# Performance work log

Measured on AMD Instinct MI355X. Metric: run time of the kernel, lower is better.

The kernel has to match this reference:

```python
import jax, jax.numpy as jnp
import numpy as np

N = 50000      # nodes
E = 500000     # directed edges
F_IN = 112     # node feature dim
G = 256        # number of graphs in batch


def _lin(key, fan_in, fan_out):
    # torch nn.Linear default init: U(-1/sqrt(fan_in), 1/sqrt(fan_in))
    s = 1.0 / np.sqrt(fan_in)
    kw, kb = jax.random.split(key)
    W = jax.random.uniform(kw, (fan_in, fan_out), jnp.float32, -s, s)
    b = jax.random.uniform(kb, (fan_out,), jnp.float32, -s, s)
    return W, b


def setup_inputs() -> dict:
    key = jax.random.key(0)
    ks = jax.random.split(key, 9)
    x = jax.random.normal(ks[0], (N, F_IN), jnp.float32)
    edge_index = jax.random.randint(ks[1], (2, E), 0, N)
    # sorted graph ids, guaranteeing every graph id 0..G-1 appears
    batch = jnp.sort(jnp.concatenate([jnp.arange(G),
                                      jax.random.randint(ks[2], (N - G,), 0, G)]))
    W1, b1 = _lin(ks[3], F_IN, 336)
    W2, b2 = _lin(ks[4], 336, 168)
    Wg, bg = _lin(ks[5], 168, 84)
    Wf, bf = _lin(ks[6], 84, 42)
    Wo, bo = _lin(ks[7], 42, 1)
    return dict(x=x, edge_index=edge_index, batch=batch,
                W1=W1, b1=b1, W2=W2, b2=b2,
                Wg=Wg, bg=bg, Wf=Wf, bf=bf, Wo=Wo, bo=bo)


def _gcn_conv(x, W, b, src, dst, n):
    """PyG GCNConv: add self-loops, symmetric D^-1/2 A D^-1/2 normalization."""
    h = x @ W                                   # [n, out]
    loop = jnp.arange(n, dtype=src.dtype)
    src_f = jnp.concatenate([src, loop])        # [E+n]
    dst_f = jnp.concatenate([dst, loop])
    deg = jax.ops.segment_sum(jnp.ones(src_f.shape[0], jnp.float32), dst_f, n)
    dinv = jnp.where(deg > 0, jax.lax.rsqrt(deg), 0.0)
    norm = dinv[src_f] * dinv[dst_f]            # [E+n]
    out = jax.ops.segment_sum(h[src_f] * norm[:, None], dst_f, n)
    return out + b


def reference(x, edge_index, batch, W1, b1, W2, b2, Wg, bg, Wf, bf, Wo, bo):
    src, dst = edge_index[0], edge_index[1]
    h = jax.nn.relu(_gcn_conv(x, W1, b1, src, dst, N))
    # dropout is identity in eval mode
    h = jax.nn.relu(_gcn_conv(h, W2, b2, src, dst, N))
    g = jax.ops.segment_max(h, batch, G)        # global max pool -> [G, 168]
    g = jax.nn.relu(g @ Wg + bg)
    g = jax.nn.relu(g @ Wf + bf)
    return g @ Wo + bo                           # [G, 1]
```

## Files before the change

### kernel.cpp

```cpp
#include <hip/hip_runtime.h>
#include <hip/hip_fp16.h>

#define N_NODES 50000
#define MPAD    50048
#define N_EDGES 500000
#define F_IN    112
#define K1P     128
#define F1      336
#define K2P     352
#define F2      168
#define NGRAPH  256
#define SCAN_CHUNK 1024
#define SCAN_BLOCKS ((N_NODES + SCAN_CHUNK - 1) / SCAN_CHUNK)

typedef __attribute__((ext_vector_type(8))) _Float16 f16x8;
typedef __attribute__((ext_vector_type(4))) float f32x4;
typedef unsigned short ushort_t;

__device__ __forceinline__ ushort_t f16_bits(float x) {
    __half h = __float2half_rn(x);
    return *(ushort_t*)&h;
}

__global__ void k_zero_int(int* p, int n) {
    int i = blockIdx.x * blockDim.x + threadIdx.x;
    if (i < n) p[i] = 0;
}

#define CVX_BLOCKS  ((N_NODES * (F_IN / 4) + 255) / 256)
#define CNT_BLOCKS  ((N_EDGES / 2 + 255) / 256)
#define CVW1_BLOCKS ((384 * K1P + 255) / 256)
#define CVW2_BLOCKS ((192 * K2P + 255) / 256)
#define RNG_BLOCKS  ((N_NODES + 255) / 256)
#define PREP_BLOCKS (CVX_BLOCKS + CNT_BLOCKS + CVW1_BLOCKS + CVW2_BLOCKS + RNG_BLOCKS)

__global__ __launch_bounds__(256) void k_prep(const float* __restrict__ x,
                                              const int* __restrict__ dst,
                                              const float* __restrict__ W1,
                                              const float* __restrict__ W2,
                                              const int* __restrict__ batch,
                                              ushort_t* __restrict__ x16,
                                              int* __restrict__ dcount,
                                              ushort_t* __restrict__ w1t,
                                              ushort_t* __restrict__ w2t,
                                              int* __restrict__ r0, int* __restrict__ r1) {
    int bid = blockIdx.x;
    int t = threadIdx.x;
    if (bid < CVX_BLOCKS) {
        int i = bid * 256 + t;
        if (i < N_NODES * (F_IN / 4)) {
            float4 v = ((const float4*)x)[i];
            __half2 h0 = __floats2half2_rn(v.x, v.y);
            __half2 h1 = __floats2half2_rn(v.z, v.w);
            uint2 u; u.x = *(unsigned*)&h0; u.y = *(unsigned*)&h1;
            ((uint2*)x16)[i] = u;
        }
        return;
    }
    bid -= CVX_BLOCKS;
    if (bid < CNT_BLOCKS) {
        int i = bid * 256 + t;
        if (i < N_EDGES / 2) {
            int2 d = ((const int2*)dst)[i];
            atomicAdd(&dcount[d.x], 1);
            atomicAdd(&dcount[d.y], 1);
        }
        return;
    }
    bid -= CNT_BLOCKS;
    if (bid < CVW1_BLOCKS) {
        int idx = bid * 256 + t;
        if (idx < 384 * K1P) {
            int n = idx / K1P, k = idx % K1P;
            float v = (n < F1 && k < F_IN) ? W1[k * F1 + n] : 0.0f;
            w1t[idx] = f16_bits(v);
        }
        return;
    }
    bid -= CVW1_BLOCKS;
    if (bid < CVW2_BLOCKS) {
        int idx = bid * 256 + t;
        if (idx < 192 * K2P) {
            int n = idx / K2P, k = idx % K2P;
            float v = (n < F2 && k < F1) ? W2[k * F2 + n] : 0.0f;
            w2t[idx] = f16_bits(v);
        }
        return;
    }
    bid -= CVW2_BLOCKS;
    {
        int v = bid * 256 + t;
        if (v >= N_NODES) return;
        int b = batch[v];
        if (v == 0 || batch[v - 1] != b) r0[b] = v;
        if (v == N_NODES - 1 || batch[v + 1] != b) r1[b] = v + 1;
    }
}

__global__ __launch_bounds__(SCAN_CHUNK) void k_scan1(const int* __restrict__ dcount,
                                                      int* __restrict__ off,
                                                      int* __restrict__ partials,
                                                      float* __restrict__ dinv, int n) {
    __shared__ int s[SCAN_CHUNK];
    int t = threadIdx.x;
    int i = blockIdx.x * SCAN_CHUNK + t;
    int val = (i < n) ? dcount[i] : 0;
    s[t] = val;
    __syncthreads();
    for (int d = 1; d < SCAN_CHUNK; d <<= 1) {
        int x = (t >= d) ? s[t - d] : 0;
        __syncthreads();
        s[t] += x;
        __syncthreads();
    }
    if (i < n) {
        off[i] = s[t] - val;
        dinv[i] = rsqrtf((float)val + 1.0f);
    }
    if (t == SCAN_CHUNK - 1) partials[blockIdx.x] = s[t];
}
__global__ __launch_bounds__(SCAN_CHUNK) void k_scan3(int* __restrict__ off,
                                                      const int* __restrict__ partials, int n) {
    __shared__ int tmp[SCAN_BLOCKS];
    __shared__ int pref[SCAN_BLOCKS];
    int t = threadIdx.x;
    if (t < SCAN_BLOCKS) tmp[t] = partials[t];
    __syncthreads();
    if (t == 0) {
        int run = 0;
        for (int j = 0; j < SCAN_BLOCKS; ++j) { pref[j] = run; run += tmp[j]; }
    }
    __syncthreads();
    int i = blockIdx.x * SCAN_CHUNK + t;
    if (i < n) off[i] += pref[blockIdx.x];
    if (i == n) off[i] = N_EDGES;
}

__global__ void k_scatter(const int* __restrict__ src, const int* __restrict__ dst,
                          const int* __restrict__ off, int* __restrict__ cur,
                          const float* __restrict__ dinv,
                          int2* __restrict__ csr, int e2) {
    int i = blockIdx.x * blockDim.x + threadIdx.x;
    if (i >= e2) return;
    int2 s2 = ((const int2*)src)[i];
    int2 d2 = ((const int2*)dst)[i];
    {
        int pos = atomicAdd(&cur[d2.x], 1);
        int2 rec; rec.x = s2.x; rec.y = __float_as_int(dinv[s2.x] * dinv[d2.x]);
        csr[off[d2.x] + pos] = rec;
    }
    {
        int pos = atomicAdd(&cur[d2.y], 1);
        int2 rec; rec.x = s2.y; rec.y = __float_as_int(dinv[s2.y] * dinv[d2.y]);
        csr[off[d2.y] + pos] = rec;
    }
}

__global__ __launch_bounds__(256) void k_agg1(const ushort_t* __restrict__ X16,
                                              const int* __restrict__ off,
                                              const int2* __restrict__ csr,
                                              const float* __restrict__ dinv,
                                              ushort_t* __restrict__ aX) {
    int w = (blockIdx.x * 256 + threadIdx.x) >> 6;
    int lane = threadIdx.x & 63;
    if (w >= N_NODES / 2) return;
    const int g = lane >> 5, sl = lane & 31;
    const int v = 2 * w + g;
    const bool act = sl < 28;
    int o0A = off[2 * w], oM = off[2 * w + 1], o1B = off[2 * w + 2];
    int o0 = g ? oM : o0A;
    int n  = g ? (o1B - oM) : (oM - o0A);
    int nmax = max(oM - o0A, o1B - oM);
    float di = dinv[v];
    float4 acc = {0, 0, 0, 0};
    if (act) {
        uint2 u = *(const uint2*)(X16 + (long)v * F_IN + sl * 4);
        float2 f0 = __half22float2(*(__half2*)&u.x);
        float2 f1 = __half22float2(*(__half2*)&u.y);
        float s2 = di * di;
        acc.x = f0.x * s2; acc.y = f0.y * s2; acc.z = f1.x * s2; acc.w = f1.y * s2;
    }
    int nm1 = max(n - 1, 0);
    for (int b = 0; b < nmax; b += 8) {
        int2 e[8];
        #pragma unroll
        for (int j = 0; j < 8; ++j) {
            int cidx = min(o0 + min(b + j, nm1), N_EDGES - 1);
            e[j] = csr[cidx];
        }
        uint2 u[8];
        #pragma unroll
        for (int j = 0; j < 8; ++j) {
            bool valid = (b + j) < n;
            int s = valid ? e[j].x : v;
            if (act) u[j] = *(const uint2*)(X16 + (long)s * F_IN + sl * 4);
        }
        #pragma unroll
        for (int j = 0; j < 8; ++j) {
            bool valid = (b + j) < n;
            float c = valid ? __int_as_float(e[j].y) : 0.0f;
            float2 f0 = __half22float2(*(__half2*)&u[j].x);
            float2 f1 = __half22float2(*(__half2*)&u[j].y);
            acc.x += c * f0.x; acc.y += c * f0.y; acc.z += c * f1.x; acc.w += c * f1.y;
        }
    }
    if (sl < 32) {
        uint2 o = {0, 0};
        if (act) {
            __half2 h0 = __floats2half2_rn(acc.x, acc.y);
            __half2 h1 = __floats2half2_rn(acc.z, acc.w);
            o.x = *(unsigned*)&h0; o.y = *(unsigned*)&h1;
        }
        *(uint2*)(aX + (long)v * K1P + sl * 4) = o;
    }
}

template<int NT, int KP, int EPI>
__global__ __launch_bounds__(256) void k_gemm_f16(
        const ushort_t* __restrict__ A, const ushort_t* __restrict__ Bt,
        const float* __restrict__ bias,
        ushort_t* __restrict__ C, int M, int Nreal, int CW) {
    constexpr int NS = NT / 32;
    __shared__ ushort_t As[64][40];
    __shared__ ushort_t Bs[NT][40];
    const int tid = threadIdx.x;
    const int row0 = blockIdx.y * 64;
    const int col0 = blockIdx.x * NT;
    const int w  = tid >> 6, l = tid & 63;
    const int wm = w >> 1, wn = w & 1;
    const int lm = l & 15, lq = l >> 4;

    f32x4 acc[2][NS];
    #pragma unroll
    for (int i = 0; i < 2; ++i)
        #pragma unroll
        for (int j = 0; j < NS; ++j) acc[i][j] = (f32x4){0.f, 0.f, 0.f, 0.f};

    const int arow  = tid >> 2;
    const int akoff = (tid & 3) * 8;

    for (int k0 = 0; k0 < KP; k0 += 32) {
        *(int4*)&As[arow][akoff] = *(const int4*)&A[(long)(row0 + arow) * KP + k0 + akoff];
        #pragma unroll
        for (int c = 0; c < NT / 64; ++c)
            *(int4*)&Bs[c * 64 + arow][akoff] =
                *(const int4*)&Bt[(long)(col0 + c * 64 + arow) * KP + k0 + akoff];
        __syncthreads();

        f16x8 af[2], bf[NS];
        #pragma unroll
        for (int ms = 0; ms < 2; ++ms)
            af[ms] = *(const f16x8*)&As[wm * 32 + ms * 16 + lm][lq * 8];
        #pragma unroll
        for (int ns = 0; ns < NS; ++ns)
            bf[ns] = *(const f16x8*)&Bs[wn * (NT / 2) + ns * 16 + lm][lq * 8];
        #pragma unroll
        for (int ms = 0; ms < 2; ++ms)
            #pragma unroll
            for (int ns = 0; ns < NS; ++ns)
                acc[ms][ns] = __builtin_amdgcn_mfma_f32_16x16x32_f16(af[ms], bf[ns], acc[ms][ns], 0, 0, 0);
        __syncthreads();
    }

    #pragma unroll
    for (int ms = 0; ms < 2; ++ms) {
        int R = row0 + wm * 32 + ms * 16 + lq * 4;
        #pragma unroll
        for (int ns = 0; ns < NS; ++ns) {
            int col = col0 + wn * (NT / 2) + ns * 16 + lm;
            if (EPI == 1) {
                if (col < CW) {
                    float bb = (col < Nreal) ? bias[col] : 0.0f;
                    #pragma unroll
                    for (int i = 0; i < 4; ++i) {
                        int row = R + i;
                        if (row < M) {
                            float r = (col < Nreal) ? fmaxf(acc[ms][ns][i] + bb, 0.0f) : 0.0f;
                            C[(long)row * CW + col] = f16_bits(r);
                        }
                    }
                }
            } else {
                if (col < Nreal) {
                    #pragma unroll
                    for (int i = 0; i < 4; ++i) {
                        int row = R + i;
                        if (row < M) C[(long)row * Nreal + col] = f16_bits(acc[ms][ns][i]);
                    }
                }
            }
        }
    }
}

__global__ __launch_bounds__(256) void k_agg2(const ushort_t* __restrict__ T16,
                                              const int* __restrict__ off,
                                              const int2* __restrict__ csr,
                                              const float* __restrict__ dinv,
                                              const float* __restrict__ b2,
                                              ushort_t* __restrict__ out2) {
    int w = (blockIdx.x * 256 + threadIdx.x) >> 6;
    int lane = threadIdx.x & 63;
    if (w >= N_NODES / 2) return;
    const int g = lane >> 5, sl = lane & 31;
    const int v = 2 * w + g;
    const bool act = sl < 21;
    int o0A = off[2 * w], oM = off[2 * w + 1], o1B = off[2 * w + 2];
    int o0 = g ? oM : o0A;
    int n  = g ? (o1B - oM) : (oM - o0A);
    int nmax = max(oM - o0A, o1B - oM);
    float di = dinv[v];
    float4 a0 = {0, 0, 0, 0}, a1 = {0, 0, 0, 0};
    if (act) {
        uint4 u = *(const uint4*)(T16 + (long)v * F2 + sl * 8);
        float2 f0 = __half22float2(*(__half2*)&u.x);
        float2 f1 = __half22float2(*(__half2*)&u.y);
        float2 f2 = __half22float2(*(__half2*)&u.z);
        float2 f3 = __half22float2(*(__half2*)&u.w);
        float s2 = di * di;
        a0.x = f0.x * s2; a0.y = f0.y * s2; a0.z = f1.x * s2; a0.w = f1.y * s2;
        a1.x = f2.x * s2; a1.y = f2.y * s2; a1.z = f3.x * s2; a1.w = f3.y * s2;
    }
    int nm1 = max(n - 1, 0);
    for (int b = 0; b < nmax; b += 8) {
        int2 e[8];
        #pragma unroll
        for (int j = 0; j < 8; ++j) {
            int cidx = min(o0 + min(b + j, nm1), N_EDGES - 1);
            e[j] = csr[cidx];
        }
        uint4 u[8];
        #pragma unroll
        for (int j = 0; j < 8; ++j) {
            bool valid = (b + j) < n;
            int s = valid ? e[j].x : v;
            if (act) u[j] = *(const uint4*)(T16 + (long)s * F2 + sl * 8);
        }
        #pragma unroll
        for (int j = 0; j < 8; ++j) {
            bool valid = (b + j) < n;
            float c = valid ? __int_as_float(e[j].y) : 0.0f;
            float2 f0 = __half22float2(*(__half2*)&u[j].x);
            float2 f1 = __half22float2(*(__half2*)&u[j].y);
            float2 f2 = __half22float2(*(__half2*)&u[j].z);
            float2 f3 = __half22float2(*(__half2*)&u[j].w);
            a0.x += c * f0.x; a0.y += c * f0.y; a0.z += c * f1.x; a0.w += c * f1.y;
            a1.x += c * f2.x; a1.y += c * f2.y; a1.z += c * f3.x; a1.w += c * f3.y;
        }
    }
    if (act) {
        float4 bb0 = ((const float4*)b2)[sl * 2];
        float4 bb1 = ((const float4*)b2)[sl * 2 + 1];
        __half2 h0 = __floats2half2_rn(fmaxf(a0.x + bb0.x, 0.0f), fmaxf(a0.y + bb0.y, 0.0f));
        __half2 h1 = __floats2half2_rn(fmaxf(a0.z + bb0.z, 0.0f), fmaxf(a0.w + bb0.w, 0.0f));
        __half2 h2 = __floats2half2_rn(fmaxf(a1.x + bb1.x, 0.0f), fmaxf(a1.y + bb1.y, 0.0f));
        __half2 h3 = __floats2half2_rn(fmaxf(a1.z + bb1.z, 0.0f), fmaxf(a1.w + bb1.w, 0.0f));
        uint4 o;
        o.x = *(unsigned*)&h0; o.y = *(unsigned*)&h1;
        o.z = *(unsigned*)&h2; o.w = *(unsigned*)&h3;
        *(uint4*)(out2 + (long)v * F2 + sl * 8) = o;
    }
}

__global__ __launch_bounds__(256) void k_pool_head(const ushort_t* __restrict__ out2,
        const int* __restrict__ r0, const int* __restrict__ r1,
        const float* __restrict__ Wg, const float* __restrict__ bg,
        const float* __restrict__ Wf, const float* __restrict__ bf,
        const float* __restrict__ Wo, const float* __restrict__ bo,
        float* __restrict__ out) {
    __shared__ float4 sm[4][F2 / 4];
    __shared__ float s0[F2];
    __shared__ float s1[84];
    __shared__ float s2[42];
    int gi = blockIdx.x;
    int slot = threadIdx.x >> 6, lane = threadIdx.x & 63;
    int a = r0[gi], b = r1[gi];
    if (lane < F2 / 4) {
        float4 mx = {0, 0, 0, 0};
        for (int v = a + slot; v < b; v += 4) {
            uint2 u = ((const uint2*)(out2 + (long)v * F2))[lane];
            float2 f0 = __half22float2(*(__half2*)&u.x);
            float2 f1 = __half22float2(*(__half2*)&u.y);
            mx.x = fmaxf(mx.x, f0.x); mx.y = fmaxf(mx.y, f0.y);
            mx.z = fmaxf(mx.z, f1.x); mx.w = fmaxf(mx.w, f1.y);
        }
        sm[slot][lane] = mx;
    }
    __syncthreads();
    if (slot == 0 && lane < F2 / 4) {
        float4 m0 = sm[0][lane], m1 = sm[1][lane], m2 = sm[2][lane], m3 = sm[3][lane];
        float4 r;
        r.x = fmaxf(fmaxf(m0.x, m1.x), fmaxf(m2.x, m3.x));
        r.y = fmaxf(fmaxf(m0.y, m1.y), fmaxf(m2.y, m3.y));
        r.z = fmaxf(fmaxf(m0.z, m1.z), fmaxf(m2.z, m3.z));
        r.w = fmaxf(fmaxf(m0.w, m1.w), fmaxf(m2.w, m3.w));
        ((float4*)s0)[lane] = r;
    }
    __syncthreads();
    int t = threadIdx.x;
    if (t < 84) {
        float acc = bg[t];
        #pragma unroll 4
        for (int k = 0; k < F2; ++k) acc += s0[k] * Wg[k * 84 + t];
        s1[t] = fmaxf(acc, 0.0f);
    }
    __syncthreads();
    if (t < 42) {
        float acc = bf[t];
        #pragma unroll 4
        for (int k = 0; k < 84; ++k) acc += s1[k] * Wf[k * 42 + t];
        s2[t] = fmaxf(acc, 0.0f);
    }
    __syncthreads();
    if (t == 0) {
        float acc = bo[0];
        for (int k = 0; k < 42; ++k) acc += s2[k] * Wo[k];
        out[gi] = acc;
    }
}

extern "C" void kernel_launch(void* const* d_in, const int* in_sizes, int n_in,
                              void* d_out, int out_size, void* d_ws, size_t ws_size,
                              hipStream_t stream) {
    const float* x   = (const float*)d_in[0];
    const int*   ei  = (const int*)d_in[1];
    const int*   bat = (const int*)d_in[2];
    const float* W1  = (const float*)d_in[3];
    const float* b1  = (const float*)d_in[4];
    const float* W2  = (const float*)d_in[5];
    const float* b2  = (const float*)d_in[6];
    const float* Wg  = (const float*)d_in[7];
    const float* bg  = (const float*)d_in[8];
    const float* Wf  = (const float*)d_in[9];
    const float* bf  = (const float*)d_in[10];
    const float* Wo  = (const float*)d_in[11];
    const float* bo  = (const float*)d_in[12];
    float* out = (float*)d_out;

    char* p = (char*)d_ws;
    float* dinv     = (float*)p; p += 50048 * 4;
    int*   dcount   = (int*)p;   p += 50048 * 4;
    int*   cur      = (int*)p;   p += 50048 * 4;
    int*   off      = (int*)p;   p += 50064 * 4;
    int*   partials = (int*)p;   p += 64 * 4;
    int*   rng0     = (int*)p;   p += 256 * 4;
    int*   rng1     = (int*)p;   p += 256 * 4;
    int2*  csr      = (int2*)p;  p += (long)N_EDGES * 8;
    ushort_t* x16   = (ushort_t*)p; p += (long)N_NODES * F_IN * 2;
    ushort_t* aX    = (ushort_t*)p; p += (long)MPAD * K1P * 2;
    ushort_t* w1t   = (ushort_t*)p; p += (long)384 * K1P * 2;
    ushort_t* w2t   = (ushort_t*)p; p += (long)192 * K2P * 2;
    ushort_t* h1    = (ushort_t*)p; p += (long)MPAD * K2P * 2;
    ushort_t* t16   = (ushort_t*)p; p += (long)N_NODES * F2 * 2;
    ushort_t* o16   = (ushort_t*)p; p += (long)N_NODES * F2 * 2;

    const int* src = ei;
    const int* dst = ei + N_EDGES;
    const int B = 256;

    k_zero_int<<<(2 * 50048 + B - 1) / B, B, 0, stream>>>(dcount, 2 * 50048);
    k_prep<<<PREP_BLOCKS, B, 0, stream>>>(x, dst, W1, W2, bat, x16, dcount, w1t, w2t, rng0, rng1);
    k_scan1<<<SCAN_BLOCKS, SCAN_CHUNK, 0, stream>>>(dcount, off, partials, dinv, N_NODES);
    k_scan3<<<SCAN_BLOCKS, SCAN_CHUNK, 0, stream>>>(off, partials, N_NODES);
    k_scatter<<<(N_EDGES / 2 + B - 1) / B, B, 0, stream>>>(src, dst, off, cur, dinv, csr, N_EDGES / 2);

    k_agg1<<<(N_NODES / 2 * 64) / 256, 256, 0, stream>>>(x16, off, csr, dinv, aX);
    dim3 gg1(3, MPAD / 64);
    k_gemm_f16<128, K1P, 1><<<gg1, 256, 0, stream>>>(aX, w1t, b1, h1, N_NODES, F1, K2P);

    dim3 gg2(1, MPAD / 64);
    k_gemm_f16<192, K2P, 2><<<gg2, 256, 0, stream>>>(h1, w2t, nullptr, t16, N_NODES, F2, 0);
    k_agg2<<<(N_NODES / 2 * 64) / 256, 256, 0, stream>>>(t16, off, csr, dinv, b2, o16);

    k_pool_head<<<NGRAPH, 256, 0, stream>>>(o16, rng0, rng1, Wg, bg, Wf, bf, Wo, bo, out);
}
```

Baseline: 290.6 us.

## Fuse both GCN GEMMs into one kernel keeping H1 in shared memory

```diff
diff --git a/kernel.cpp b/kernel.cpp
--- a/kernel.cpp
+++ b/kernel.cpp
@@ -9,6 +9,7 @@
 #define F1      336
 #define K2P     352
 #define F2      168
+#define T2W     192
 #define NGRAPH  256
 #define SCAN_CHUNK 1024
 #define SCAN_BLOCKS ((N_NODES + SCAN_CHUNK - 1) / SCAN_CHUNK)
@@ -27,7 +28,7 @@
     if (i < n) p[i] = 0;
 }
 
-#define CVX_BLOCKS  ((N_NODES * (F_IN / 4) + 255) / 256)
+#define CVX_BLOCKS  ((N_NODES * 32) / 256)
 #define CNT_BLOCKS  ((N_EDGES / 2 + 255) / 256)
 #define CVW1_BLOCKS ((384 * K1P + 255) / 256)
 #define CVW2_BLOCKS ((192 * K2P + 255) / 256)
@@ -48,13 +49,15 @@
     int t = threadIdx.x;
     if (bid < CVX_BLOCKS) {
         int i = bid * 256 + t;
-        if (i < N_NODES * (F_IN / 4)) {
-            float4 v = ((const float4*)x)[i];
-            __half2 h0 = __floats2half2_rn(v.x, v.y);
-            __half2 h1 = __floats2half2_rn(v.z, v.w);
-            uint2 u; u.x = *(unsigned*)&h0; u.y = *(unsigned*)&h1;
-            ((uint2*)x16)[i] = u;
-        }
+        int v = i >> 5, c = i & 31;
+        uint2 u = {0, 0};
+        if (c < 28) {
+            float4 f = *(const float4*)&x[(long)v * F_IN + c * 4];
+            __half2 h0 = __floats2half2_rn(f.x, f.y);
+            __half2 h1 = __floats2half2_rn(f.z, f.w);
+            u.x = *(unsigned*)&h0; u.y = *(unsigned*)&h1;
+        }
+        ((uint2*)x16)[i] = u;
         return;
     }
     bid -= CVX_BLOCKS;
@@ -166,131 +169,136 @@
     if (w >= N_NODES / 2) return;
     const int g = lane >> 5, sl = lane & 31;
     const int v = 2 * w + g;
-    const bool act = sl < 28;
     int o0A = off[2 * w], oM = off[2 * w + 1], o1B = off[2 * w + 2];
     int o0 = g ? oM : o0A;
     int n  = g ? (o1B - oM) : (oM - o0A);
     int nmax = max(oM - o0A, o1B - oM);
     float di = dinv[v];
-    float4 acc = {0, 0, 0, 0};
-    if (act) {
-        uint2 u = *(const uint2*)(X16 + (long)v * F_IN + sl * 4);
-        float2 f0 = __half22float2(*(__half2*)&u.x);
-        float2 f1 = __half22float2(*(__half2*)&u.y);
-        float s2 = di * di;
-        acc.x = f0.x * s2; acc.y = f0.y * s2; acc.z = f1.x * s2; acc.w = f1.y * s2;
-    }
+    float s2 = di * di;
+    uint2 us = *(const uint2*)(X16 + (long)v * K1P + sl * 4);
+    float2 sf0 = __half22float2(*(__half2*)&us.x);
+    float2 sf1 = __half22float2(*(__half2*)&us.y);
+    float4 acc = {sf0.x * s2, sf0.y * s2, sf1.x * s2, sf1.y * s2};
     int nm1 = max(n - 1, 0);
-    for (int b = 0; b < nmax; b += 8) {
-        int2 e[8];
-        #pragma unroll
-        for (int j = 0; j < 8; ++j) {
+    for (int b = 0; b < nmax; b += 16) {
+        int2 e[16];
+        #pragma unroll
+        for (int j = 0; j < 16; ++j) {
             int cidx = min(o0 + min(b + j, nm1), N_EDGES - 1);
             e[j] = csr[cidx];
         }
-        uint2 u[8];
-        #pragma unroll
-        for (int j = 0; j < 8; ++j) {
-            bool valid = (b + j) < n;
-            int s = valid ? e[j].x : v;
-            if (act) u[j] = *(const uint2*)(X16 + (long)s * F_IN + sl * 4);
-        }
-        #pragma unroll
-        for (int j = 0; j < 8; ++j) {
-            bool valid = (b + j) < n;
-            float c = valid ? __int_as_float(e[j].y) : 0.0f;
+        uint2 u[16];
+        #pragma unroll
+        for (int j = 0; j < 16; ++j)
+            u[j] = *(const uint2*)(X16 + (long)e[j].x * K1P + sl * 4);
+        #pragma unroll
+        for (int j = 0; j < 16; ++j) {
+            float c = ((b + j) < n) ? __int_as_float(e[j].y) : 0.0f;
             float2 f0 = __half22float2(*(__half2*)&u[j].x);
             float2 f1 = __half22float2(*(__half2*)&u[j].y);
             acc.x += c * f0.x; acc.y += c * f0.y; acc.z += c * f1.x; acc.w += c * f1.y;
         }
     }
-    if (sl < 32) {
-        uint2 o = {0, 0};
-        if (act) {
-            __half2 h0 = __floats2half2_rn(acc.x, acc.y);
-            __half2 h1 = __floats2half2_rn(acc.z, acc.w);
-            o.x = *(unsigned*)&h0; o.y = *(unsigned*)&h1;
-        }
-        *(uint2*)(aX + (long)v * K1P + sl * 4) = o;
-    }
-}
-
-template<int NT, int KP, int EPI>
-__global__ __launch_bounds__(256) void k_gemm_f16(
-        const ushort_t* __restrict__ A, const ushort_t* __restrict__ Bt,
-        const float* __restrict__ bias,
-        ushort_t* __restrict__ C, int M, int Nreal, int CW) {
-    constexpr int NS = NT / 32;
+    __half2 h0 = __floats2half2_rn(acc.x, acc.y);
+    __half2 h1 = __floats2half2_rn(acc.z, acc.w);
+    uint2 o; o.x = *(unsigned*)&h0; o.y = *(unsigned*)&h1;
+    *(uint2*)(aX + (long)v * K1P + sl * 4) = o;
+}
+
+__global__ __launch_bounds__(256) void k_gemm_fused(
+        const ushort_t* __restrict__ aX,
+        const ushort_t* __restrict__ w1t,
+        const float* __restrict__ b1,
+        const ushort_t* __restrict__ w2t,
+        ushort_t* __restrict__ T2) {
     __shared__ ushort_t As[64][40];
-    __shared__ ushort_t Bs[NT][40];
+    __shared__ ushort_t Bs[352][40];
+    __shared__ ushort_t H1s[64][360];
     const int tid = threadIdx.x;
-    const int row0 = blockIdx.y * 64;
-    const int col0 = blockIdx.x * NT;
-    const int w  = tid >> 6, l = tid & 63;
+    const int row0 = blockIdx.x * 64;
+    const int w = tid >> 6, l = tid & 63;
     const int wm = w >> 1, wn = w & 1;
     const int lm = l & 15, lq = l >> 4;
 
-    f32x4 acc[2][NS];
+    f32x4 acc1[2][11];
     #pragma unroll
     for (int i = 0; i < 2; ++i)
         #pragma unroll
-        for (int j = 0; j < NS; ++j) acc[i][j] = (f32x4){0.f, 0.f, 0.f, 0.f};
-
-    const int arow  = tid >> 2;
-    const int akoff = (tid & 3) * 8;
-
-    for (int k0 = 0; k0 < KP; k0 += 32) {
-        *(int4*)&As[arow][akoff] = *(const int4*)&A[(long)(row0 + arow) * KP + k0 + akoff];
-        #pragma unroll
-        for (int c = 0; c < NT / 64; ++c)
-            *(int4*)&Bs[c * 64 + arow][akoff] =
-                *(const int4*)&Bt[(long)(col0 + c * 64 + arow) * KP + k0 + akoff];
-        __syncthreads();
-
-        f16x8 af[2], bf[NS];
-        #pragma unroll
-        for (int ms = 0; ms < 2; ++ms)
-            af[ms] = *(const f16x8*)&As[wm * 32 + ms * 16 + lm][lq * 8];
-        #pragma unroll
-        for (int ns = 0; ns < NS; ++ns)
-            bf[ns] = *(const f16x8*)&Bs[wn * (NT / 2) + ns * 16 + lm][lq * 8];
-        #pragma unroll
-        for (int ms = 0; ms < 2; ++ms)
+        for (int j = 0; j < 11; ++j) acc1[i][j] = (f32x4){0.f, 0.f, 0.f, 0.f};
+
+    for (int k0 = 0; k0 < K1P; k0 += 32) {
+        {
+            int r = tid >> 2, s = (tid & 3) * 8;
+            *(int4*)&As[r][s] = *(const int4*)&aX[(long)(row0 + r) * K1P + k0 + s];
+        }
+        #pragma unroll
+        for (int it = 0; it < 6; ++it) {
+            int f = tid + it * 256;
+            if (f < 1408) {
+                int r = f >> 2, s = (f & 3) * 8;
+                *(int4*)&Bs[r][s] = *(const int4*)&w1t[(long)r * K1P + k0 + s];
+            }
+        }
+        __syncthreads();
+        f16x8 af0 = *(const f16x8*)&As[wm * 32 + lm][lq * 8];
+        f16x8 af1 = *(const f16x8*)&As[wm * 32 + 16 + lm][lq * 8];
+        #pragma unroll
+        for (int ns = 0; ns < 11; ++ns) {
+            f16x8 bf = *(const f16x8*)&Bs[wn * 176 + ns * 16 + lm][lq * 8];
+            acc1[0][ns] = __builtin_amdgcn_mfma_f32_16x16x32_f16(af0, bf, acc1[0][ns], 0, 0, 0);
+            acc1[1][ns] = __builtin_amdgcn_mfma_f32_16x16x32_f16(af1, bf, acc1[1][ns], 0, 0, 0);
+        }
+        __syncthreads();
+    }
+    #pragma unroll
+    for (int ms = 0; ms < 2; ++ms)
+        #pragma unroll
+        for (int ns = 0; ns < 11; ++ns) {
+            int col = wn * 176 + ns * 16 + lm;
+            float bb = (col < F1) ? b1[col] : 0.0f;
             #pragma unroll
-            for (int ns = 0; ns < NS; ++ns)
-                acc[ms][ns] = __builtin_amdgcn_mfma_f32_16x16x32_f16(af[ms], bf[ns], acc[ms][ns], 0, 0, 0);
-        __syncthreads();
-    }
-
+            for (int i = 0; i < 4; ++i) {
+                int r = wm * 32 + ms * 16 + lq * 4 + i;
+                H1s[r][col] = f16_bits(fmaxf(acc1[ms][ns][i] + bb, 0.0f));
+            }
+        }
+    __syncthreads();
+
+    f32x4 acc2[2][6];
     #pragma unroll
-    for (int ms = 0; ms < 2; ++ms) {
-        int R = row0 + wm * 32 + ms * 16 + lq * 4;
-        #pragma unroll
-        for (int ns = 0; ns < NS; ++ns) {
-            int col = col0 + wn * (NT / 2) + ns * 16 + lm;
-            if (EPI == 1) {
-                if (col < CW) {
-                    float bb = (col < Nreal) ? bias[col] : 0.0f;
-                    #pragma unroll
-                    for (int i = 0; i < 4; ++i) {
-                        int row = R + i;
-                        if (row < M) {
-                            float r = (col < Nreal) ? fmaxf(acc[ms][ns][i] + bb, 0.0f) : 0.0f;
-                            C[(long)row * CW + col] = f16_bits(r);
-                        }
-                    }
-                }
-            } else {
-                if (col < Nreal) {
-                    #pragma unroll
-                    for (int i = 0; i < 4; ++i) {
-                        int row = R + i;
-                        if (row < M) C[(long)row * Nreal + col] = f16_bits(acc[ms][ns][i]);
-                    }
-                }
+    for (int i = 0; i < 2; ++i)
+        #pragma unroll
+        for (int j = 0; j < 6; ++j) acc2[i][j] = (f32x4){0.f, 0.f, 0.f, 0.f};
+
+    for (int k0 = 0; k0 < K2P; k0 += 32) {
+        #pragma unroll
+        for (int it = 0; it < 3; ++it) {
+            int f = tid + it * 256;
+            int r = f >> 2, s = (f & 3) * 8;
+            *(int4*)&Bs[r][s] = *(const int4*)&w2t[(long)r * K2P + k0 + s];
+        }
+        __syncthreads();
+        f16x8 af0 = *(const f16x8*)&H1s[wm * 32 + lm][k0 + lq * 8];
+        f16x8 af1 = *(const f16x8*)&H1s[wm * 32 + 16 + lm][k0 + lq * 8];
+        #pragma unroll
+        for (int ns = 0; ns < 6; ++ns) {
+            f16x8 bf = *(const f16x8*)&Bs[wn * 96 + ns * 16 + lm][lq * 8];
+            acc2[0][ns] = __builtin_amdgcn_mfma_f32_16x16x32_f16(af0, bf, acc2[0][ns], 0, 0, 0);
+            acc2[1][ns] = __builtin_amdgcn_mfma_f32_16x16x32_f16(af1, bf, acc2[1][ns], 0, 0, 0);
+        }
+        __syncthreads();
+    }
+    #pragma unroll
+    for (int ms = 0; ms < 2; ++ms)
+        #pragma unroll
+        for (int ns = 0; ns < 6; ++ns) {
+            int col = wn * 96 + ns * 16 + lm;
+            #pragma unroll
+            for (int i = 0; i < 4; ++i) {
+                int r = row0 + wm * 32 + ms * 16 + lq * 4 + i;
+                T2[(long)r * T2W + col] = f16_bits(acc2[ms][ns][i]);
             }
         }
-    }
 }
 
 __global__ __launch_bounds__(256) void k_agg2(const ushort_t* __restrict__ T16,
@@ -312,7 +320,7 @@
     float di = dinv[v];
     float4 a0 = {0, 0, 0, 0}, a1 = {0, 0, 0, 0};
     if (act) {
-        uint4 u = *(const uint4*)(T16 + (long)v * F2 + sl * 8);
+        uint4 u = *(const uint4*)(T16 + (long)v * T2W + sl * 8);
         float2 f0 = __half22float2(*(__half2*)&u.x);
         float2 f1 = __half22float2(*(__half2*)&u.y);
         float2 f2 = __half22float2(*(__half2*)&u.z);
@@ -322,24 +330,22 @@
         a1.x = f2.x * s2; a1.y = f2.y * s2; a1.z = f3.x * s2; a1.w = f3.y * s2;
     }
     int nm1 = max(n - 1, 0);
-    for (int b = 0; b < nmax; b += 8) {
-        int2 e[8];
-        #pragma unroll
-        for (int j = 0; j < 8; ++j) {
+    for (int b = 0; b < nmax; b += 16) {
+        int2 e[16];
+        #pragma unroll
+        for (int j = 0; j < 16; ++j) {
             int cidx = min(o0 + min(b + j, nm1), N_EDGES - 1);
             e[j] = csr[cidx];
         }
-        uint4 u[8];
-        #pragma unroll
-        for (int j = 0; j < 8; ++j) {
-            bool valid = (b + j) < n;
-            int s = valid ? e[j].x : v;
-            if (act) u[j] = *(const uint4*)(T16 + (long)s * F2 + sl * 8);
-        }
-        #pragma unroll
-        for (int j = 0; j < 8; ++j) {
-            bool valid = (b + j) < n;
-            float c = valid ? __int_as_float(e[j].y) : 0.0f;
+        uint4 u[16];
+        #pragma unroll
+        for (int j = 0; j < 16; ++j) {
+            int s = ((b + j) < n) ? e[j].x : v;
+            if (act) u[j] = *(const uint4*)(T16 + (long)s * T2W + sl * 8);
+        }
+        #pragma unroll
+        for (int j = 0; j < 16; ++j) {
+            float c = ((b + j) < n) ? __int_as_float(e[j].y) : 0.0f;
             float2 f0 = __half22float2(*(__half2*)&u[j].x);
             float2 f1 = __half22float2(*(__half2*)&u[j].y);
             float2 f2 = __half22float2(*(__half2*)&u[j].z);
@@ -446,12 +452,11 @@
     int*   rng0     = (int*)p;   p += 256 * 4;
     int*   rng1     = (int*)p;   p += 256 * 4;
     int2*  csr      = (int2*)p;  p += (long)N_EDGES * 8;
-    ushort_t* x16   = (ushort_t*)p; p += (long)N_NODES * F_IN * 2;
+    ushort_t* x16   = (ushort_t*)p; p += (long)N_NODES * K1P * 2;
     ushort_t* aX    = (ushort_t*)p; p += (long)MPAD * K1P * 2;
     ushort_t* w1t   = (ushort_t*)p; p += (long)384 * K1P * 2;
     ushort_t* w2t   = (ushort_t*)p; p += (long)192 * K2P * 2;
-    ushort_t* h1    = (ushort_t*)p; p += (long)MPAD * K2P * 2;
-    ushort_t* t16   = (ushort_t*)p; p += (long)N_NODES * F2 * 2;
+    ushort_t* t16   = (ushort_t*)p; p += (long)MPAD * T2W * 2;
     ushort_t* o16   = (ushort_t*)p; p += (long)N_NODES * F2 * 2;
 
     const int* src = ei;
@@ -465,11 +470,8 @@
     k_scatter<<<(N_EDGES / 2 + B - 1) / B, B, 0, stream>>>(src, dst, off, cur, dinv, csr, N_EDGES / 2);
 
     k_agg1<<<(N_NODES / 2 * 64) / 256, 256, 0, stream>>>(x16, off, csr, dinv, aX);
-    dim3 gg1(3, MPAD / 64);
-    k_gemm_f16<128, K1P, 1><<<gg1, 256, 0, stream>>>(aX, w1t, b1, h1, N_NODES, F1, K2P);
-
-    dim3 gg2(1, MPAD / 64);
-    k_gemm_f16<192, K2P, 2><<<gg2, 256, 0, stream>>>(h1, w2t, nullptr, t16, N_NODES, F2, 0);
+    k_gemm_fused<<<MPAD / 64, 256, 0, stream>>>(aX, w1t, b1, w2t, t16);
+
     k_agg2<<<(N_NODES / 2 * 64) / 256, 256, 0, stream>>>(t16, off, csr, dinv, b2, o16);
 
     k_pool_head<<<NGRAPH, 256, 0, stream>>>(o16, rng0, rng1, Wg, bg, Wf, bf, Wo, bo, out);
```

Result: faster. 284.5 us (-2.1%).
